# Performance work log

Hardware: AMD Instinct MI355X
Metric: run time of the kernel (lower is better)

The kernel has to match this reference:

```python
import jax, jax.numpy as jnp
import numpy as np

B, O, L, E = 8, 4, 1024, 1024
BETA = 512
NSEG = 12
OUT = 1


def setup_inputs() -> dict:
    key = jax.random.key(0)
    ks = jax.random.split(key, 8)
    hidden = jax.random.normal(ks[0], (B, O, L, E), jnp.float32)
    # strictly increasing boundaries in (1, L), shared across the O options (as in the torch code)
    raw = jnp.sort(jax.random.randint(ks[1], (B, NSEG), 2, L - NSEG), axis=-1)
    idx = raw + jnp.arange(NSEG, dtype=raw.dtype)
    s = 0.02
    Wp = jax.random.normal(ks[2], (E, 2 * BETA), jnp.float32) * s
    bp = jnp.zeros((2 * BETA,), jnp.float32)
    Wa0 = jax.random.normal(ks[3], (2 * BETA, BETA), jnp.float32) * s
    ba0 = jnp.zeros((BETA,), jnp.float32)
    Wa = jax.random.normal(ks[4], (BETA, BETA), jnp.float32) * s
    ba = jnp.zeros((BETA,), jnp.float32)
    Wl0 = jax.random.normal(ks[5], (8 * BETA, BETA), jnp.float32) * s
    bl0 = jnp.zeros((BETA,), jnp.float32)
    Wl = jax.random.normal(ks[6], (BETA, OUT), jnp.float32) * s
    bl = jnp.zeros((OUT,), jnp.float32)
    return dict(hidden=hidden, idx=idx, Wp=Wp, bp=bp, Wa0=Wa0, ba0=ba0,
                Wa=Wa, ba=ba, Wl0=Wl0, bl0=bl0, Wl=Wl, bl=bl)


def _seg_mean(P, starts, ends):
    # P: [B,O,L+1,E] exclusive prefix sums; starts/ends: [B,K] token offsets.
    s = jnp.take_along_axis(P, starts[:, None, :, None], axis=2)
    e = jnp.take_along_axis(P, ends[:, None, :, None], axis=2)
    cnt = (ends - starts).astype(P.dtype)[:, None, :, None]
    return (e - s) / cnt  # [B,O,K,E]


def _get_param(x, Wp, bp):
    e = 1.0 + jax.nn.relu(x @ Wp + bp)
    a, b = jnp.split(e, 2, axis=-1)
    return a, b


def _attn_pool(a, b, Wa0, ba0, Wa, ba):
    # attention-weighted reduction over axis -2 (the 'logic' operator)
    h = jax.nn.relu(jnp.concatenate([a, b], axis=-1) @ Wa0 + ba0)
    w = jax.nn.softmax(h @ Wa + ba, axis=-2)
    return (w * a).sum(axis=-2), (w * b).sum(axis=-2)


def reference(hidden, idx, Wp, bp, Wa0, ba0, Wa, ba, Wl0, bl0, Wl, bl):
    # ---- init_embed: ragged segment means via prefix sums (one pass, no host syncs)
    P = jnp.concatenate([jnp.zeros_like(hidden[:, :, :1]),
                         jnp.cumsum(hidden, axis=2)], axis=2)  # [B,O,L+1,E]
    ones = jnp.ones((idx.shape[0], 1), idx.dtype)
    starts_c = jnp.concatenate([ones, idx[:, :NSEG - 3]], axis=1)  # [B, NSEG-2]
    ends_c = idx[:, :NSEG - 2]
    ctx = _seg_mean(P, starts_c, ends_c)                                # [B,O,Nc,E]
    q = _seg_mean(P, idx[:, NSEG - 3:NSEG - 2], idx[:, NSEG - 2:NSEG - 1])[:, :, 0]
    o = _seg_mean(P, idx[:, NSEG - 2:NSEG - 1], idx[:, NSEG - 1:NSEG])[:, :, 0]
    allc = _seg_mean(P, ones, idx[:, NSEG - 3:NSEG - 2])[:, :, 0]       # [B,O,E]
    # ---- beta params for context segments
    a_c, b_c = _get_param(ctx, Wp, bp)                                  # [B,O,Nc,BETA]
    # intersection over segments
    ia, ib = _attn_pool(a_c, b_c, Wa0, ba0, Wa, ba)                     # [B,O,BETA]
    # renew: pair each segment with the intersection, pool over the pair axis
    pa = jnp.stack([a_c, jnp.broadcast_to(ia[:, :, None, :], a_c.shape)], axis=-2)
    pb = jnp.stack([b_c, jnp.broadcast_to(ib[:, :, None, :], b_c.shape)], axis=-2)
    na, nb = _attn_pool(pa, pb, Wa0, ba0, Wa, ba)                       # [B,O,Nc,BETA]
    # union: invert, attention-pool over segments, invert back
    ua, ub = _attn_pool(1.0 / na, 1.0 / nb, Wa0, ba0, Wa, ba)
    ua, ub = 1.0 / ua, 1.0 / ub                                         # [B,O,BETA]
    # ---- beta params for question / option / whole-context spans
    a_q, b_q = _get_param(q, Wp, bp)
    a_o, b_o = _get_param(o, Wp, bp)
    a_ac, b_ac = _get_param(allc, Wp, bp)
    # ---- classify head: concat 4 beta embeddings -> 8*BETA -> MLP -> logits
    cat = jnp.concatenate([ua, ub, a_ac, b_ac, a_o, b_o, a_q, b_q], axis=-1)
    h = jax.nn.relu(cat @ Wl0 + bl0)
    return h @ Wl + bl  # [B,O,OUT]
```

## Files before the change

### kernel.cpp

```cpp
#include <hip/hip_runtime.h>
#include <hip/hip_bf16.h>

#define B_    8
#define O_    4
#define L_    1024
#define E_    1024
#define BETA_ 512
#define NSEG_ 12
#define BO_   32

enum : size_t {
  WS_S    = 0,
  WS_P1   = WS_S   + (size_t)BO_ * 12 * E_,
  WS_H1   = WS_P1  + (size_t)BO_ * 13 * E_,
  WS_T1   = WS_H1  + (size_t)BO_ * 10 * BETA_,
  WS_H2   = WS_T1  + (size_t)BO_ * 10 * BETA_,
  WS_T2   = WS_H2  + (size_t)BO_ * BETA_,
  WS_H3   = WS_T2  + (size_t)BO_ * BETA_,
  WS_T3   = WS_H3  + (size_t)BO_ * 10 * BETA_,
  WS_HF   = WS_T3  + (size_t)BO_ * 10 * BETA_,
  WS_ZEND = WS_HF  + (size_t)BO_ * BETA_,
  WS_IAB  = WS_ZEND,
  WS_RN   = WS_IAB + (size_t)BO_ * 2 * BETA_,
  WS_END  = WS_RN  + (size_t)BO_ * 10 * E_,
};

__device__ __forceinline__ float relu_(float v) { return v > 0.f ? v : 0.f; }

__global__ void k1_segsum(const float* __restrict__ hidden, const int* __restrict__ idx,
                          float* __restrict__ S) {
    const int bo = blockIdx.y;
    const int b = bo >> 2;
    int cuts[13];
    cuts[0] = 1;
#pragma unroll
    for (int i = 0; i < 12; ++i) cuts[i + 1] = idx[b * NSEG_ + i];
    const int rows = L_ / 64;
    const int l0 = blockIdx.x * rows;
    const int l1 = l0 + rows;
    int lo = l0 < 1 ? 1 : l0;
    const int hi = l1 < cuts[12] ? l1 : cuts[12];
    if (lo >= hi) return;
    const int e4 = threadIdx.x << 2;
    const float* base = hidden + (size_t)bo * (L_ * E_) + e4;
    int j = 0;
    while (j < 11 && cuts[j + 1] <= lo) ++j;
    int l = lo;
    while (l < hi) {
        const int e2 = (j < 11 && cuts[j + 1] < hi) ? cuts[j + 1] : hi;
        float sx = 0.f, sy = 0.f, sz = 0.f, sw = 0.f;
        for (; l < e2; ++l) {
            const float4 v = *reinterpret_cast<const float4*>(base + (size_t)l * E_);
            sx += v.x; sy += v.y; sz += v.z; sw += v.w;
        }
        float* sp = S + ((size_t)bo * 12 + j) * E_ + e4;
        atomicAdd(sp + 0, sx);
        atomicAdd(sp + 1, sy);
        atomicAdd(sp + 2, sz);
        atomicAdd(sp + 3, sw);
        ++j;
    }
}

template<int M, int K, int N, int KC, int BOG, int XF, int XBO>
__global__ __launch_bounds__(256) void gemm_sk(
    const float* __restrict__ Xb, const float* __restrict__ xbias,
    const float* __restrict__ W, float* __restrict__ OUT,
    const float* __restrict__ A0, const float* __restrict__ A1,
    const float* __restrict__ A2, const float* __restrict__ A3,
    const float* __restrict__ A4, const float* __restrict__ A5,
    float* __restrict__ SIDE, const int* __restrict__ idxp) {
    const int k0  = blockIdx.x * KC;
    const int bo0 = blockIdx.y * BOG;
    const int c   = blockIdx.z * 256 + threadIdx.x;
    const int tid = threadIdx.x;
    __shared__ __align__(16) float xs[BOG * M * KC];

    float invc[12], invall;
    if constexpr (XF == 3) {
        int cuts[13];
        cuts[0] = 1;
        const int b0 = bo0 >> 2;
#pragma unroll
        for (int i = 0; i < 12; ++i) cuts[i + 1] = idxp[b0 * NSEG_ + i];
#pragma unroll
        for (int m = 0; m < 12; ++m) invc[m] = 1.0f / (float)(cuts[m + 1] - cuts[m]);
        invall = 1.0f / (float)(cuts[10] - 1);
    }

    for (int i = tid; i < BOG * M * KC; i += 256) {
        const int kk = i % KC;
        const int rm = i / KC;
        const int m  = rm % M;
        const int bb = rm / M;
        const int bo = bo0 + bb;
        const int k  = k0 + kk;
        float v;
        if constexpr (XF == 0) {
            v = Xb[(size_t)bo * XBO + (size_t)m * K + k];
        } else if constexpr (XF == 1 || XF == 2) {
            v = Xb[(size_t)bo * XBO + (size_t)m * K + k] + xbias[k];
            v = relu_(v);
            if constexpr (XF == 1) v += 1.f;
        } else if constexpr (XF == 3) {
            if (m < 12) {
                v = Xb[((size_t)bo * 12 + m) * E_ + k] * invc[m];
            } else {
                float s = 0.f;
#pragma unroll
                for (int r = 0; r < 10; ++r) s += Xb[((size_t)bo * 12 + r) * E_ + k];
                v = s * invall;
            }
        } else if constexpr (XF == 4) {
            const int col = k & 511, half = k >> 9;
            const float bac = A2[col];
            float t[10], mx = -1e30f;
#pragma unroll
            for (int j = 0; j < 10; ++j) {
                t[j] = A0[((size_t)bo * 10 + j) * BETA_ + col] + bac;
                mx = fmaxf(mx, t[j]);
            }
            float p[10], sw = 0.f;
#pragma unroll
            for (int j = 0; j < 10; ++j) { p[j] = expf(t[j] - mx); sw += p[j]; }
            const float bpc = A3[half * BETA_ + col];
            float acc = 0.f;
#pragma unroll
            for (int j = 0; j < 10; ++j) {
                const float e = 1.f + relu_(A1[(size_t)bo * 13 * E_ + (size_t)j * E_ + half * BETA_ + col] + bpc);
                acc = fmaf(p[j], e, acc);
            }
            v = acc / sw;
            SIDE[(size_t)bo * 1024 + k] = v;
        } else if constexpr (XF == 5) {
            const int col = k & 511, half = k >> 9;
            const int j = m;
            const float bac = A4[col];
            const float tj = A0[((size_t)bo * 10 + j) * BETA_ + col] + bac;
            const float tI = A1[(size_t)bo * BETA_ + col] + bac;
            const float mx = fmaxf(tj, tI);
            const float e0 = expf(tj - mx);
            const float e1 = expf(tI - mx);
            const float iv = A2[(size_t)bo * 1024 + half * BETA_ + col];
            const float ea = 1.f + relu_(A3[(size_t)bo * 13 * E_ + (size_t)j * E_ + half * BETA_ + col] + A5[half * BETA_ + col]);
            v = (e0 + e1) / (e0 * ea + e1 * iv);
            SIDE[((size_t)bo * 10 + j) * 1024 + k] = v;
        } else {
            if (k < 1024) {
                const int col = k & 511, half = k >> 9;
                const float bac = A3[col];
                float t[10], mx = -1e30f;
#pragma unroll
                for (int j = 0; j < 10; ++j) {
                    t[j] = A0[((size_t)bo * 10 + j) * BETA_ + col] + bac;
                    mx = fmaxf(mx, t[j]);
                }
                float sw = 0.f, acc = 0.f;
#pragma unroll
                for (int j = 0; j < 10; ++j) {
                    const float p = expf(t[j] - mx);
                    sw += p;
                    acc = fmaf(p, A1[((size_t)bo * 10 + j) * 1024 + half * BETA_ + col], acc);
                }
                v = sw / acc;
            } else {
                const int region = k >> 10;
                const int row = (region == 1) ? 12 : (region == 2) ? 11 : 10;
                const int col = k & 1023;
                v = 1.f + relu_(A2[(size_t)bo * 13 * E_ + (size_t)row * E_ + col] + A4[col]);
            }
        }
        xs[i] = v;
    }
    __syncthreads();

    float acc[BOG][M];
#pragma unroll
    for (int b = 0; b < BOG; ++b)
#pragma unroll
        for (int m = 0; m < M; ++m) acc[b][m] = 0.f;
    const float* __restrict__ wp = W + (size_t)k0 * N + c;
    for (int k4 = 0; k4 < KC / 4; ++k4) {
        const float w0 = wp[(size_t)(4 * k4 + 0) * N];
        const float w1 = wp[(size_t)(4 * k4 + 1) * N];
        const float w2 = wp[(size_t)(4 * k4 + 2) * N];
        const float w3 = wp[(size_t)(4 * k4 + 3) * N];
#pragma unroll
        for (int b = 0; b < BOG; ++b) {
#pragma unroll
            for (int m = 0; m < M; ++m) {
                const float4 xv = *reinterpret_cast<const float4*>(&xs[(b * M + m) * KC + 4 * k4]);
                float a = acc[b][m];
                a = fmaf(xv.x, w0, a);
                a = fmaf(xv.y, w1, a);
                a = fmaf(xv.z, w2, a);
                a = fmaf(xv.w, w3, a);
                acc[b][m] = a;
            }
        }
    }
#pragma unroll
    for (int b = 0; b < BOG; ++b) {
        float* op = OUT + (size_t)(bo0 + b) * M * N + c;
#pragma unroll
        for (int m = 0; m < M; ++m) atomicAdd(op + (size_t)m * N, acc[b][m]);
    }
}

__global__ void __launch_bounds__(512) k_final(
    const float* __restrict__ HF, const float* __restrict__ bl0,
    const float* __restrict__ Wl, const float* __restrict__ bl,
    float* __restrict__ out) {
    const int bo = blockIdx.x;
    const int c = threadIdx.x;
    const float v1 = relu_(HF[(size_t)bo * BETA_ + c] + bl0[c]) * Wl[c];
    const float v2 = relu_(HF[(size_t)bo * BETA_ + 256 + c] + bl0[256 + c]) * Wl[256 + c];
    float partial = v1 + v2;
#pragma unroll
    for (int off = 32; off > 0; off >>= 1) partial += __shfl_down(partial, off, 64);
    __shared__ float red[8];
    if ((c & 63) == 0) red[c >> 6] = partial;
    __syncthreads();
    if (c == 0) out[bo] = red[0] + red[1] + red[2] + red[3] + bl[0];
}

extern "C" void kernel_launch(void* const* d_in, const int* in_sizes, int n_in,
                              void* d_out, int out_size, void* d_ws, size_t ws_size,
                              hipStream_t stream) {
    const float* hidden = (const float*)d_in[0];
    const int* idx = (const int*)d_in[1];
    const float* Wp  = (const float*)d_in[2];
    const float* bp  = (const float*)d_in[3];
    const float* Wa0 = (const float*)d_in[4];
    const float* ba0 = (const float*)d_in[5];
    const float* Wa  = (const float*)d_in[6];
    const float* ba  = (const float*)d_in[7];
    const float* Wl0 = (const float*)d_in[8];
    const float* bl0 = (const float*)d_in[9];
    const float* Wl  = (const float*)d_in[10];
    const float* bl  = (const float*)d_in[11];
    float* ws = (float*)d_ws;
    float* S   = ws + WS_S;
    float* P1  = ws + WS_P1;
    float* H1  = ws + WS_H1;
    float* T1  = ws + WS_T1;
    float* H2  = ws + WS_H2;
    float* T2  = ws + WS_T2;
    float* H3  = ws + WS_H3;
    float* T3  = ws + WS_T3;
    float* HF  = ws + WS_HF;
    float* IAB = ws + WS_IAB;
    float* RN  = ws + WS_RN;
    const float* NUL = nullptr;

    hipMemsetAsync(S, 0, (size_t)WS_ZEND * sizeof(float), stream);
    k1_segsum<<<dim3(64, BO_), 256, 0, stream>>>(hidden, idx, S);
    gemm_sk<13, 1024, 1024, 128, 2, 3, 0>
        <<<dim3(8, 16, 4), 256, 0, stream>>>(S, NUL, Wp, P1, NUL, NUL, NUL, NUL, NUL, NUL, nullptr, idx);
    gemm_sk<10, 1024, 512, 64, 2, 1, 13 * 1024>
        <<<dim3(16, 16, 2), 256, 0, stream>>>(P1, bp, Wa0, H1, NUL, NUL, NUL, NUL, NUL, NUL, nullptr, nullptr);
    gemm_sk<10, 512, 512, 64, 2, 2, 10 * 512>
        <<<dim3(8, 16, 2), 256, 0, stream>>>(H1, ba0, Wa, T1, NUL, NUL, NUL, NUL, NUL, NUL, nullptr, nullptr);
    gemm_sk<1, 1024, 512, 128, 8, 4, 0>
        <<<dim3(8, 4, 2), 256, 0, stream>>>(NUL, NUL, Wa0, H2, T1, P1, ba, bp, NUL, NUL, IAB, nullptr);
    gemm_sk<1, 512, 512, 64, 8, 2, 512>
        <<<dim3(8, 4, 2), 256, 0, stream>>>(H2, ba0, Wa, T2, NUL, NUL, NUL, NUL, NUL, NUL, nullptr, nullptr);
    gemm_sk<10, 1024, 512, 64, 2, 5, 0>
        <<<dim3(16, 16, 2), 256, 0, stream>>>(NUL, NUL, Wa0, H3, T1, T2, IAB, P1, ba, bp, RN, nullptr);
    gemm_sk<10, 512, 512, 64, 2, 2, 10 * 512>
        <<<dim3(8, 16, 2), 256, 0, stream>>>(H3, ba0, Wa, T3, NUL, NUL, NUL, NUL, NUL, NUL, nullptr, nullptr);
    gemm_sk<1, 4096, 512, 128, 8, 6, 0>
        <<<dim3(32, 4, 2), 256, 0, stream>>>(NUL, NUL, Wl0, HF, T3, RN, P1, ba, bp, NUL, nullptr, nullptr);
    k_final<<<BO_, 512, 0, stream>>>(HF, bl0, Wl, bl, (float*)d_out);
}
```

Before: 189.4 us.

## Replace atomic split-K accumulation with partial buffers reduced by consumers

Every split-K GEMM and the segment-sum kernel now write per-chunk partial results to separate workspace slices with plain stores, and the next stage sums those partials while loading its input. This removes the large memset and all float atomicAdds. It also adds a small means kernel and caches the 1+relu(P1) and T1 values so later stages can reuse them. In exchange, consumer loads read more data (up to 32 partials) and the workspace grows.

Measured after the change: 164.9 us. 1.15x faster.

```diff
diff --git a/kernel.cpp b/kernel.cpp
--- a/kernel.cpp
+++ b/kernel.cpp
@@ -8,40 +8,47 @@
 #define BETA_ 512
 #define NSEG_ 12
 #define BO_   32
+#define NCH_  16
 
 enum : size_t {
-  WS_S    = 0,
-  WS_P1   = WS_S   + (size_t)BO_ * 12 * E_,
-  WS_H1   = WS_P1  + (size_t)BO_ * 13 * E_,
-  WS_T1   = WS_H1  + (size_t)BO_ * 10 * BETA_,
-  WS_H2   = WS_T1  + (size_t)BO_ * 10 * BETA_,
-  WS_T2   = WS_H2  + (size_t)BO_ * BETA_,
-  WS_H3   = WS_T2  + (size_t)BO_ * BETA_,
-  WS_T3   = WS_H3  + (size_t)BO_ * 10 * BETA_,
-  WS_HF   = WS_T3  + (size_t)BO_ * 10 * BETA_,
-  WS_ZEND = WS_HF  + (size_t)BO_ * BETA_,
-  WS_IAB  = WS_ZEND,
-  WS_RN   = WS_IAB + (size_t)BO_ * 2 * BETA_,
-  WS_END  = WS_RN  + (size_t)BO_ * 10 * E_,
+  WS_SPART = 0,
+  WS_X     = WS_SPART + (size_t)BO_ * NCH_ * 12 * E_,
+  WS_P1P   = WS_X     + (size_t)BO_ * 13 * E_,
+  WS_H1P   = WS_P1P   + (size_t)8  * BO_ * 13 * E_,
+  WS_T1P   = WS_H1P   + (size_t)16 * BO_ * 10 * BETA_,
+  WS_H2P   = WS_T1P   + (size_t)8  * BO_ * 10 * BETA_,
+  WS_T2P   = WS_H2P   + (size_t)8  * BO_ * BETA_,
+  WS_H3P   = WS_T2P   + (size_t)8  * BO_ * BETA_,
+  WS_T3P   = WS_H3P   + (size_t)16 * BO_ * 10 * BETA_,
+  WS_HFP   = WS_T3P   + (size_t)8  * BO_ * 10 * BETA_,
+  WS_TE    = WS_HFP   + (size_t)32 * BO_ * BETA_,
+  WS_T1B   = WS_TE    + (size_t)BO_ * 13 * E_,
+  WS_IAB   = WS_T1B   + (size_t)BO_ * 10 * BETA_,
+  WS_RN    = WS_IAB   + (size_t)BO_ * 2 * BETA_,
+  WS_END   = WS_RN    + (size_t)BO_ * 10 * E_,
 };
 
 __device__ __forceinline__ float relu_(float v) { return v > 0.f ? v : 0.f; }
 
 __global__ void k1_segsum(const float* __restrict__ hidden, const int* __restrict__ idx,
-                          float* __restrict__ S) {
+                          float* __restrict__ Spart) {
+    const int chunk = blockIdx.x;
     const int bo = blockIdx.y;
     const int b = bo >> 2;
     int cuts[13];
     cuts[0] = 1;
 #pragma unroll
     for (int i = 0; i < 12; ++i) cuts[i + 1] = idx[b * NSEG_ + i];
-    const int rows = L_ / 64;
-    const int l0 = blockIdx.x * rows;
-    const int l1 = l0 + rows;
+    const int e4 = threadIdx.x << 2;
+    float* sp = Spart + ((size_t)(bo * NCH_ + chunk) * 12) * E_ + e4;
+    const float4 z = make_float4(0.f, 0.f, 0.f, 0.f);
+#pragma unroll
+    for (int m = 0; m < 12; ++m) *reinterpret_cast<float4*>(sp + (size_t)m * E_) = z;
+    const int l0 = chunk * 64;
+    const int l1 = l0 + 64;
     int lo = l0 < 1 ? 1 : l0;
     const int hi = l1 < cuts[12] ? l1 : cuts[12];
     if (lo >= hi) return;
-    const int e4 = threadIdx.x << 2;
     const float* base = hidden + (size_t)bo * (L_ * E_) + e4;
     int j = 0;
     while (j < 11 && cuts[j + 1] <= lo) ++j;
@@ -53,121 +60,139 @@
             const float4 v = *reinterpret_cast<const float4*>(base + (size_t)l * E_);
             sx += v.x; sy += v.y; sz += v.z; sw += v.w;
         }
-        float* sp = S + ((size_t)bo * 12 + j) * E_ + e4;
-        atomicAdd(sp + 0, sx);
-        atomicAdd(sp + 1, sy);
-        atomicAdd(sp + 2, sz);
-        atomicAdd(sp + 3, sw);
+        float4 s; s.x = sx; s.y = sy; s.z = sz; s.w = sw;
+        *reinterpret_cast<float4*>(sp + (size_t)j * E_) = s;
         ++j;
     }
 }
 
-template<int M, int K, int N, int KC, int BOG, int XF, int XBO>
+__global__ __launch_bounds__(256) void k2_means(
+    const float* __restrict__ Spart, const int* __restrict__ idx,
+    float* __restrict__ X) {
+    const int bo = blockIdx.y;
+    const int col = blockIdx.x * 256 + threadIdx.x;
+    const int b = bo >> 2;
+    int cuts[13];
+    cuts[0] = 1;
+#pragma unroll
+    for (int i = 0; i < 12; ++i) cuts[i + 1] = idx[b * NSEG_ + i];
+    const float* sp = Spart + (size_t)bo * NCH_ * 12 * E_ + col;
+    float allc = 0.f;
+#pragma unroll
+    for (int m = 0; m < 12; ++m) {
+        float s = 0.f;
+#pragma unroll
+        for (int ch = 0; ch < NCH_; ++ch) s += sp[((size_t)ch * 12 + m) * E_];
+        X[((size_t)bo * 13 + m) * E_ + col] = s / (float)(cuts[m + 1] - cuts[m]);
+        if (m < 10) allc += s;
+    }
+    X[((size_t)bo * 13 + 12) * E_ + col] = allc / (float)(cuts[10] - 1);
+}
+
+template<int M, int ML, int K, int N, int KC, int BOG, int XF, int NPART>
 __global__ __launch_bounds__(256) void gemm_sk(
     const float* __restrict__ Xb, const float* __restrict__ xbias,
     const float* __restrict__ W, float* __restrict__ OUT,
     const float* __restrict__ A0, const float* __restrict__ A1,
     const float* __restrict__ A2, const float* __restrict__ A3,
-    const float* __restrict__ A4, const float* __restrict__ A5,
-    float* __restrict__ SIDE, const int* __restrict__ idxp) {
-    const int k0  = blockIdx.x * KC;
+    float* __restrict__ SIDE, float* __restrict__ SIDE2) {
+    const int kidx = blockIdx.x;
+    const int k0 = kidx * KC;
     const int bo0 = blockIdx.y * BOG;
-    const int c   = blockIdx.z * 256 + threadIdx.x;
+    const int c = blockIdx.z * 256 + threadIdx.x;
     const int tid = threadIdx.x;
-    __shared__ __align__(16) float xs[BOG * M * KC];
-
-    float invc[12], invall;
-    if constexpr (XF == 3) {
-        int cuts[13];
-        cuts[0] = 1;
-        const int b0 = bo0 >> 2;
-#pragma unroll
-        for (int i = 0; i < 12; ++i) cuts[i + 1] = idxp[b0 * NSEG_ + i];
-#pragma unroll
-        for (int m = 0; m < 12; ++m) invc[m] = 1.0f / (float)(cuts[m + 1] - cuts[m]);
-        invall = 1.0f / (float)(cuts[10] - 1);
-    }
-
-    for (int i = tid; i < BOG * M * KC; i += 256) {
+    __shared__ __align__(16) float xs[BOG * ML * KC];
+
+    for (int i = tid; i < BOG * ML * KC; i += 256) {
         const int kk = i % KC;
         const int rm = i / KC;
-        const int m  = rm % M;
-        const int bb = rm / M;
+        const int m = rm % ML;
+        const int bb = rm / ML;
         const int bo = bo0 + bb;
-        const int k  = k0 + kk;
+        const int k = k0 + kk;
         float v;
         if constexpr (XF == 0) {
-            v = Xb[(size_t)bo * XBO + (size_t)m * K + k];
-        } else if constexpr (XF == 1 || XF == 2) {
-            v = Xb[(size_t)bo * XBO + (size_t)m * K + k] + xbias[k];
-            v = relu_(v);
-            if constexpr (XF == 1) v += 1.f;
-        } else if constexpr (XF == 3) {
-            if (m < 12) {
-                v = Xb[((size_t)bo * 12 + m) * E_ + k] * invc[m];
-            } else {
-                float s = 0.f;
-#pragma unroll
-                for (int r = 0; r < 10; ++r) s += Xb[((size_t)bo * 12 + r) * E_ + k];
-                v = s * invall;
-            }
+            v = Xb[((size_t)bo * ML + m) * K + k];
+        } else if constexpr (XF == 1) {
+            float s = xbias[k];
+#pragma unroll
+            for (int p = 0; p < NPART; ++p)
+                s += Xb[(((size_t)p * BO_ + bo) * ML + m) * K + k];
+            v = 1.f + relu_(s);
+            SIDE[((size_t)bo * ML + m) * K + k] = v;
+        } else if constexpr (XF == 2) {
+            float s = xbias[k];
+#pragma unroll
+            for (int p = 0; p < NPART; ++p)
+                s += Xb[(((size_t)p * BO_ + bo) * ML + m) * K + k];
+            v = relu_(s);
         } else if constexpr (XF == 4) {
             const int col = k & 511, half = k >> 9;
             const float bac = A2[col];
             float t[10], mx = -1e30f;
 #pragma unroll
             for (int j = 0; j < 10; ++j) {
-                t[j] = A0[((size_t)bo * 10 + j) * BETA_ + col] + bac;
-                mx = fmaxf(mx, t[j]);
-            }
-            float p[10], sw = 0.f;
-#pragma unroll
-            for (int j = 0; j < 10; ++j) { p[j] = expf(t[j] - mx); sw += p[j]; }
-            const float bpc = A3[half * BETA_ + col];
-            float acc = 0.f;
+                float s = bac;
+#pragma unroll
+                for (int p = 0; p < NPART; ++p)
+                    s += A0[(((size_t)p * BO_ + bo) * 10 + j) * BETA_ + col];
+                t[j] = s;
+                mx = fmaxf(mx, s);
+            }
+            if (half == 0) {
+#pragma unroll
+                for (int j = 0; j < 10; ++j)
+                    SIDE2[((size_t)bo * 10 + j) * BETA_ + col] = t[j];
+            }
+            float sw = 0.f, acc = 0.f;
 #pragma unroll
             for (int j = 0; j < 10; ++j) {
-                const float e = 1.f + relu_(A1[(size_t)bo * 13 * E_ + (size_t)j * E_ + half * BETA_ + col] + bpc);
-                acc = fmaf(p[j], e, acc);
+                const float pj = expf(t[j] - mx);
+                sw += pj;
+                acc = fmaf(pj, A1[((size_t)bo * 13 + j) * E_ + half * BETA_ + col], acc);
             }
             v = acc / sw;
             SIDE[(size_t)bo * 1024 + k] = v;
         } else if constexpr (XF == 5) {
             const int col = k & 511, half = k >> 9;
-            const int j = m;
-            const float bac = A4[col];
-            const float tj = A0[((size_t)bo * 10 + j) * BETA_ + col] + bac;
-            const float tI = A1[(size_t)bo * BETA_ + col] + bac;
+            const float tj = A0[((size_t)bo * 10 + m) * BETA_ + col];
+            float tI = A2[col];
+#pragma unroll
+            for (int p = 0; p < NPART; ++p)
+                tI += A1[((size_t)p * BO_ + bo) * BETA_ + col];
             const float mx = fmaxf(tj, tI);
             const float e0 = expf(tj - mx);
             const float e1 = expf(tI - mx);
-            const float iv = A2[(size_t)bo * 1024 + half * BETA_ + col];
-            const float ea = 1.f + relu_(A3[(size_t)bo * 13 * E_ + (size_t)j * E_ + half * BETA_ + col] + A5[half * BETA_ + col]);
+            const float ea = A3[((size_t)bo * 13 + m) * E_ + half * BETA_ + col];
+            const float iv = SIDE2[(size_t)bo * 1024 + k];
             v = (e0 + e1) / (e0 * ea + e1 * iv);
-            SIDE[((size_t)bo * 10 + j) * 1024 + k] = v;
+            SIDE[((size_t)bo * 10 + m) * E_ + k] = v;
         } else {
             if (k < 1024) {
                 const int col = k & 511, half = k >> 9;
-                const float bac = A3[col];
+                const float bac = A2[col];
                 float t[10], mx = -1e30f;
 #pragma unroll
                 for (int j = 0; j < 10; ++j) {
-                    t[j] = A0[((size_t)bo * 10 + j) * BETA_ + col] + bac;
-                    mx = fmaxf(mx, t[j]);
+                    float s = bac;
+#pragma unroll
+                    for (int p = 0; p < NPART; ++p)
+                        s += A0[(((size_t)p * BO_ + bo) * 10 + j) * BETA_ + col];
+                    t[j] = s;
+                    mx = fmaxf(mx, s);
                 }
                 float sw = 0.f, acc = 0.f;
 #pragma unroll
                 for (int j = 0; j < 10; ++j) {
-                    const float p = expf(t[j] - mx);
-                    sw += p;
-                    acc = fmaf(p, A1[((size_t)bo * 10 + j) * 1024 + half * BETA_ + col], acc);
+                    const float pj = expf(t[j] - mx);
+                    sw += pj;
+                    acc = fmaf(pj, A1[((size_t)bo * 10 + j) * E_ + k], acc);
                 }
                 v = sw / acc;
             } else {
                 const int region = k >> 10;
                 const int row = (region == 1) ? 12 : (region == 2) ? 11 : 10;
-                const int col = k & 1023;
-                v = 1.f + relu_(A2[(size_t)bo * 13 * E_ + (size_t)row * E_ + col] + A4[col]);
+                v = A3[((size_t)bo * 13 + row) * E_ + (k & 1023)];
             }
         }
         xs[i] = v;
@@ -189,7 +214,7 @@
         for (int b = 0; b < BOG; ++b) {
 #pragma unroll
             for (int m = 0; m < M; ++m) {
-                const float4 xv = *reinterpret_cast<const float4*>(&xs[(b * M + m) * KC + 4 * k4]);
+                const float4 xv = *reinterpret_cast<const float4*>(&xs[(b * ML + m) * KC + 4 * k4]);
                 float a = acc[b][m];
                 a = fmaf(xv.x, w0, a);
                 a = fmaf(xv.y, w1, a);
@@ -201,27 +226,28 @@
     }
 #pragma unroll
     for (int b = 0; b < BOG; ++b) {
-        float* op = OUT + (size_t)(bo0 + b) * M * N + c;
-#pragma unroll
-        for (int m = 0; m < M; ++m) atomicAdd(op + (size_t)m * N, acc[b][m]);
+        float* op = OUT + (((size_t)kidx * BO_ + bo0 + b) * M) * N + c;
+#pragma unroll
+        for (int m = 0; m < M; ++m) op[(size_t)m * N] = acc[b][m];
     }
 }
 
 __global__ void __launch_bounds__(512) k_final(
-    const float* __restrict__ HF, const float* __restrict__ bl0,
+    const float* __restrict__ HFP, const float* __restrict__ bl0,
     const float* __restrict__ Wl, const float* __restrict__ bl,
     float* __restrict__ out) {
     const int bo = blockIdx.x;
     const int c = threadIdx.x;
-    const float v1 = relu_(HF[(size_t)bo * BETA_ + c] + bl0[c]) * Wl[c];
-    const float v2 = relu_(HF[(size_t)bo * BETA_ + 256 + c] + bl0[256 + c]) * Wl[256 + c];
-    float partial = v1 + v2;
+    float s = bl0[c];
+#pragma unroll
+    for (int p = 0; p < 32; ++p) s += HFP[((size_t)p * BO_ + bo) * BETA_ + c];
+    float partial = relu_(s) * Wl[c];
 #pragma unroll
     for (int off = 32; off > 0; off >>= 1) partial += __shfl_down(partial, off, 64);
     __shared__ float red[8];
     if ((c & 63) == 0) red[c >> 6] = partial;
     __syncthreads();
-    if (c == 0) out[bo] = red[0] + red[1] + red[2] + red[3] + bl[0];
+    if (c == 0) out[bo] = red[0] + red[1] + red[2] + red[3] + red[4] + red[5] + red[6] + red[7] + bl[0];
 }
 
 extern "C" void kernel_launch(void* const* d_in, const int* in_sizes, int n_in,
@@ -240,36 +266,39 @@
     const float* Wl  = (const float*)d_in[10];
     const float* bl  = (const float*)d_in[11];
     float* ws = (float*)d_ws;
-    float* S   = ws + WS_S;
-    float* P1  = ws + WS_P1;
-    float* H1  = ws + WS_H1;
-    float* T1  = ws + WS_T1;
-    float* H2  = ws + WS_H2;
-    float* T2  = ws + WS_T2;
-    float* H3  = ws + WS_H3;
-    float* T3  = ws + WS_T3;
-    float* HF  = ws + WS_HF;
-    float* IAB = ws + WS_IAB;
-    float* RN  = ws + WS_RN;
+    float* SPART = ws + WS_SPART;
+    float* X     = ws + WS_X;
+    float* P1P   = ws + WS_P1P;
+    float* H1P   = ws + WS_H1P;
+    float* T1P   = ws + WS_T1P;
+    float* H2P   = ws + WS_H2P;
+    float* T2P   = ws + WS_T2P;
+    float* H3P   = ws + WS_H3P;
+    float* T3P   = ws + WS_T3P;
+    float* HFP   = ws + WS_HFP;
+    float* TE    = ws + WS_TE;
+    float* T1B   = ws + WS_T1B;
+    float* IAB   = ws + WS_IAB;
+    float* RN    = ws + WS_RN;
     const float* NUL = nullptr;
 
-    hipMemsetAsync(S, 0, (size_t)WS_ZEND * sizeof(float), stream);
-    k1_segsum<<<dim3(64, BO_), 256, 0, stream>>>(hidden, idx, S);
-    gemm_sk<13, 1024, 1024, 128, 2, 3, 0>
-        <<<dim3(8, 16, 4), 256, 0, stream>>>(S, NUL, Wp, P1, NUL, NUL, NUL, NUL, NUL, NUL, nullptr, idx);
-    gemm_sk<10, 1024, 512, 64, 2, 1, 13 * 1024>
-        <<<dim3(16, 16, 2), 256, 0, stream>>>(P1, bp, Wa0, H1, NUL, NUL, NUL, NUL, NUL, NUL, nullptr, nullptr);
-    gemm_sk<10, 512, 512, 64, 2, 2, 10 * 512>
-        <<<dim3(8, 16, 2), 256, 0, stream>>>(H1, ba0, Wa, T1, NUL, NUL, NUL, NUL, NUL, NUL, nullptr, nullptr);
-    gemm_sk<1, 1024, 512, 128, 8, 4, 0>
-        <<<dim3(8, 4, 2), 256, 0, stream>>>(NUL, NUL, Wa0, H2, T1, P1, ba, bp, NUL, NUL, IAB, nullptr);
-    gemm_sk<1, 512, 512, 64, 8, 2, 512>
-        <<<dim3(8, 4, 2), 256, 0, stream>>>(H2, ba0, Wa, T2, NUL, NUL, NUL, NUL, NUL, NUL, nullptr, nullptr);
-    gemm_sk<10, 1024, 512, 64, 2, 5, 0>
-        <<<dim3(16, 16, 2), 256, 0, stream>>>(NUL, NUL, Wa0, H3, T1, T2, IAB, P1, ba, bp, RN, nullptr);
-    gemm_sk<10, 512, 512, 64, 2, 2, 10 * 512>
-        <<<dim3(8, 16, 2), 256, 0, stream>>>(H3, ba0, Wa, T3, NUL, NUL, NUL, NUL, NUL, NUL, nullptr, nullptr);
-    gemm_sk<1, 4096, 512, 128, 8, 6, 0>
-        <<<dim3(32, 4, 2), 256, 0, stream>>>(NUL, NUL, Wl0, HF, T3, RN, P1, ba, bp, NUL, nullptr, nullptr);
-    k_final<<<BO_, 512, 0, stream>>>(HF, bl0, Wl, bl, (float*)d_out);
-}
+    k1_segsum<<<dim3(NCH_, BO_), 256, 0, stream>>>(hidden, idx, SPART);
+    k2_means<<<dim3(4, BO_), 256, 0, stream>>>(SPART, idx, X);
+    gemm_sk<13, 13, 1024, 1024, 128, 2, 0, 1>
+        <<<dim3(8, 16, 4), 256, 0, stream>>>(X, NUL, Wp, P1P, NUL, NUL, NUL, NUL, nullptr, nullptr);
+    gemm_sk<10, 13, 1024, 512, 64, 2, 1, 8>
+        <<<dim3(16, 16, 2), 256, 0, stream>>>(P1P, bp, Wa0, H1P, NUL, NUL, NUL, NUL, TE, nullptr);
+    gemm_sk<10, 10, 512, 512, 64, 2, 2, 16>
+        <<<dim3(8, 16, 2), 256, 0, stream>>>(H1P, ba0, Wa, T1P, NUL, NUL, NUL, NUL, nullptr, nullptr);
+    gemm_sk<1, 1, 1024, 512, 128, 8, 4, 8>
+        <<<dim3(8, 4, 2), 256, 0, stream>>>(NUL, NUL, Wa0, H2P, T1P, TE, ba, NUL, IAB, T1B);
+    gemm_sk<1, 1, 512, 512, 64, 8, 2, 8>
+        <<<dim3(8, 4, 2), 256, 0, stream>>>(H2P, ba0, Wa, T2P, NUL, NUL, NUL, NUL, nullptr, nullptr);
+    gemm_sk<10, 10, 1024, 512, 64, 2, 5, 8>
+        <<<dim3(16, 16, 2), 256, 0, stream>>>(NUL, NUL, Wa0, H3P, T1B, T2P, ba, TE, RN, IAB);
+    gemm_sk<10, 10, 512, 512, 64, 2, 2, 16>
+        <<<dim3(8, 16, 2), 256, 0, stream>>>(H3P, ba0, Wa, T3P, NUL, NUL, NUL, NUL, nullptr, nullptr);
+    gemm_sk<1, 1, 4096, 512, 128, 8, 6, 8>
+        <<<dim3(32, 4, 2), 256, 0, stream>>>(NUL, NUL, Wl0, HFP, T3P, RN, ba, TE, nullptr, nullptr);
+    k_final<<<BO_, 512, 0, stream>>>(HFP, bl0, Wl, bl, (float*)d_out);
+}
```
